# Performance work log

Hardware: AMD Instinct MI355X
Metric: run time of the kernel (lower is better)

The kernel has to match this reference:

```python
import jax, jax.numpy as jnp
import numpy as np

ALPHA_U = 1.0 / 10.0   # dt/tauu
ALPHA_V = 1.0 / 150.0  # dt/tauv
M = 10.0

def setup_inputs() -> dict:
    key = jax.random.key(0)
    ks = jax.random.split(key, 6)
    B, D_in, H = 8192, 1024, 2048
    stdv = 1.0 / np.sqrt(H)
    return {
        "x": jax.random.normal(ks[0], (B, D_in), dtype=jnp.float32),
        "u": jax.random.normal(ks[1], (B, H), dtype=jnp.float32),
        "v": jax.random.normal(ks[2], (B, H), dtype=jnp.float32),
        "win": jax.random.uniform(ks[3], (H, D_in), dtype=jnp.float32, minval=-stdv, maxval=stdv),
        "wr": jax.random.uniform(ks[4], (H, H), dtype=jnp.float32, minval=-stdv, maxval=stdv),
        "bias": jax.random.uniform(ks[5], (H,), dtype=jnp.float32, minval=-stdv, maxval=stdv),
    }

def reference(x, u, v, win, wr, bias):
    # v update: leaky blend toward m*u, then relu
    v_new = jax.nn.relu((1.0 - ALPHA_V) * v + (ALPHA_V * M) * u)
    # u update: leaky blend with input + recurrent drive minus adapted v
    drive = jnp.einsum('bi,hi->bh', x, win) + jnp.einsum('bk,hk->bh', u, wr) + bias - v_new
    u_new = jax.nn.relu((1.0 - ALPHA_U) * u + ALPHA_U * drive)
    return (u_new, v_new)
```

## Files before the change

kernel.cpp:

```cpp
#include <hip/hip_runtime.h>
#include <hip/hip_bf16.h>
#include <stdint.h>

#define B_DIM 8192
#define D_IN  1024
#define H_DIM 2048
#define K_DIM (D_IN + H_DIM)

#define CV_CONST  (1.0f - 1.0f/150.0f)
#define CUV_CONST (10.0f/150.0f)
#define CU_CONST  0.9f
#define AU_CONST  0.1f

typedef __attribute__((ext_vector_type(8))) short short8;
typedef __attribute__((ext_vector_type(4))) float floatx4;

__device__ __forceinline__ unsigned short f2bf(float f) {
    union { float f; unsigned u; } x; x.f = f;
    unsigned r = x.u + 0x7fffu + ((x.u >> 16) & 1u);
    return (unsigned short)(r >> 16);
}

#define N4_X   ((B_DIM * D_IN)  / 4)
#define N4_U   ((B_DIM * H_DIM) / 4)
#define N4_WIN ((H_DIM * D_IN)  / 4)
#define N4_WR  ((H_DIM * H_DIM) / 4)
#define N4_TOT (N4_X + N4_U + N4_WIN + N4_WR)

__global__ __launch_bounds__(256)
void pack_all(const float4* __restrict__ x, const float4* __restrict__ u,
              const float4* __restrict__ win, const float4* __restrict__ wr,
              unsigned short* __restrict__ Abf, unsigned short* __restrict__ Wbf) {
    int i = blockIdx.x * 256 + threadIdx.x;
    const float4* src; unsigned short* dst; int shift, mask, coloff;
    if (i < N4_X)                    { src = x;   dst = Abf; shift = 10; mask = 1023; coloff = 0;    }
    else if (i < N4_X + N4_U)        { i -= N4_X; src = u;   dst = Abf; shift = 11; mask = 2047; coloff = D_IN; }
    else if (i < N4_X + N4_U + N4_WIN){ i -= N4_X + N4_U; src = win; dst = Wbf; shift = 10; mask = 1023; coloff = 0; }
    else                             { i -= N4_X + N4_U + N4_WIN; src = wr; dst = Wbf; shift = 11; mask = 2047; coloff = D_IN; }
    int idx = i << 2;
    int r = idx >> shift;
    int c = idx & mask;
    float4 f = src[i];
    ushort4 o;
    o.x = f2bf(f.x); o.y = f2bf(f.y); o.z = f2bf(f.z); o.w = f2bf(f.w);
    *(ushort4*)(dst + (size_t)r * K_DIM + coloff + c) = o;
}

#define GLOAD_LDS16(gp, lp)                                                          \
    __builtin_amdgcn_global_load_lds(                                                \
        (const __attribute__((address_space(1))) unsigned int*)(gp),                 \
        (__attribute__((address_space(3))) unsigned int*)(lp), 16, 0, 0)

#define VMCNT(n)  asm volatile("s_waitcnt vmcnt(" #n ")" ::: "memory")
#define LGKM0     asm volatile("s_waitcnt lgkmcnt(0)" ::: "memory")
#define SCHEDB    __builtin_amdgcn_sched_barrier(0)
#define BAR       __builtin_amdgcn_s_barrier()
#define PRIO1     __builtin_amdgcn_s_setprio(1)
#define PRIO0     __builtin_amdgcn_s_setprio(0)

#define NT (K_DIM / 64)

#define ALO 0
#define BLO 16384
#define BHI 32768
#define AHI 49152

#define ES_STRIDE 68
#define ES_REGION (16 * ES_STRIDE)

__global__ __launch_bounds__(512, 2)
void gemm_fused(const unsigned short* __restrict__ A,
                const unsigned short* __restrict__ Wc,
                const float* __restrict__ u_in,
                const float* __restrict__ v_in,
                const float* __restrict__ bias,
                float* __restrict__ out)
{
    __shared__ __align__(16) unsigned char smem[131072];

    const int tid  = threadIdx.x;
    const int wave = tid >> 6;
    const int lane = tid & 63;
    const int wrh  = wave >> 2;
    const int wc   = wave & 3;

    const int bid   = blockIdx.x;
    const int xcd   = bid & 7;
    const int ord   = bid >> 3;
    const int tileM = ((xcd << 2) + (ord & 3)) << 8;
    const int tileN = (ord >> 2) << 8;

    const int frow = lane & 15;
    const int g    = lane >> 4;

    const unsigned short* Ag = A  + (size_t)(tileM + (wave >> 1) * 16 + frow) * K_DIM
                                  + (wave & 1) * 32 + g * 8;
    const unsigned short* Bg = Wc + (size_t)(tileN + (wave >> 2) * 64 + ((wave >> 1) & 1) * 16 + frow) * K_DIM
                                  + (wave & 1) * 32 + g * 8;
    const size_t R128 = (size_t)128 * K_DIM;
    const size_t R64  = (size_t) 64 * K_DIM;
    const size_t R32  = (size_t) 32 * K_DIM;

    const int w1024 = wave << 10;

    const int aRd = (wrh << 13) + (lane << 4);
    const int bRd = (wc  << 12) + (lane << 4);

    GLOAD_LDS16(Ag,               smem + ALO + w1024);
    GLOAD_LDS16(Ag + R128,        smem + ALO + 8192 + w1024);
    GLOAD_LDS16(Bg,               smem + BLO + w1024);
    GLOAD_LDS16(Bg + R128,        smem + BLO + 8192 + w1024);
    GLOAD_LDS16(Bg + R32,         smem + BHI + w1024);
    GLOAD_LDS16(Bg + R32 + R128,  smem + BHI + 8192 + w1024);
    GLOAD_LDS16(Ag + R64,         smem + AHI + w1024);
    GLOAD_LDS16(Ag + R64 + R128,  smem + AHI + 8192 + w1024);

    VMCNT(4);
    BAR;
    LGKM0;

    floatx4 acc[8][4] = {};
    short8 Ar[4][2], Bl[2][2], Bh[2][2];

#define RD_A(cb, unit, i2s) (*(const short8*)(smem + (cb) + (unit) + aRd + (i2s) * 1024))
#define RD_B(cb, unit, j2s) (*(const short8*)(smem + (cb) + (unit) + bRd + (j2s) * 1024))

#pragma clang loop unroll(disable)
    for (int t = 0; t < NT - 1; ++t) {
        const int cb = (t & 1) << 16;
        const int nb = cb ^ 65536;
        const size_t kk = (size_t)(t + 1) * 64;

        GLOAD_LDS16(Ag + kk,        smem + nb + ALO + w1024);
        GLOAD_LDS16(Ag + kk + R128, smem + nb + ALO + 8192 + w1024);
#pragma unroll
        for (int i = 0; i < 4; ++i) { Ar[i][0] = RD_A(cb, ALO, i*2); Ar[i][1] = RD_A(cb, ALO, i*2+1); }
#pragma unroll
        for (int j = 0; j < 2; ++j) { Bl[j][0] = RD_B(cb, BLO, j*2); Bl[j][1] = RD_B(cb, BLO, j*2+1); }
        VMCNT(4);
        BAR; LGKM0; SCHEDB;
        PRIO1;
#pragma unroll
        for (int i = 0; i < 4; ++i)
#pragma unroll
            for (int j = 0; j < 2; ++j) {
                acc[i][j] = __builtin_amdgcn_mfma_f32_16x16x32_bf16(Ar[i][0], Bl[j][0], acc[i][j], 0, 0, 0);
                acc[i][j] = __builtin_amdgcn_mfma_f32_16x16x32_bf16(Ar[i][1], Bl[j][1], acc[i][j], 0, 0, 0);
            }
        PRIO0; SCHEDB; BAR;

        GLOAD_LDS16(Bg + kk,        smem + nb + BLO + w1024);
        GLOAD_LDS16(Bg + kk + R128, smem + nb + BLO + 8192 + w1024);
#pragma unroll
        for (int j = 0; j < 2; ++j) { Bh[j][0] = RD_B(cb, BHI, j*2); Bh[j][1] = RD_B(cb, BHI, j*2+1); }
        VMCNT(4);
        BAR; LGKM0; SCHEDB;
        PRIO1;
#pragma unroll
        for (int i = 0; i < 4; ++i)
#pragma unroll
            for (int j = 0; j < 2; ++j) {
                acc[i][2+j] = __builtin_amdgcn_mfma_f32_16x16x32_bf16(Ar[i][0], Bh[j][0], acc[i][2+j], 0, 0, 0);
                acc[i][2+j] = __builtin_amdgcn_mfma_f32_16x16x32_bf16(Ar[i][1], Bh[j][1], acc[i][2+j], 0, 0, 0);
            }
        PRIO0; SCHEDB; BAR;

        GLOAD_LDS16(Bg + kk + R32,        smem + nb + BHI + w1024);
        GLOAD_LDS16(Bg + kk + R32 + R128, smem + nb + BHI + 8192 + w1024);
#pragma unroll
        for (int i = 0; i < 4; ++i) { Ar[i][0] = RD_A(cb, AHI, i*2); Ar[i][1] = RD_A(cb, AHI, i*2+1); }
        BAR; LGKM0; SCHEDB;
        PRIO1;
#pragma unroll
        for (int i = 0; i < 4; ++i)
#pragma unroll
            for (int j = 0; j < 2; ++j) {
                acc[4+i][2+j] = __builtin_amdgcn_mfma_f32_16x16x32_bf16(Ar[i][0], Bh[j][0], acc[4+i][2+j], 0, 0, 0);
                acc[4+i][2+j] = __builtin_amdgcn_mfma_f32_16x16x32_bf16(Ar[i][1], Bh[j][1], acc[4+i][2+j], 0, 0, 0);
            }
        PRIO0; SCHEDB; BAR;

        GLOAD_LDS16(Ag + kk + R64,        smem + nb + AHI + w1024);
        GLOAD_LDS16(Ag + kk + R64 + R128, smem + nb + AHI + 8192 + w1024);
        VMCNT(4);
        BAR; LGKM0; SCHEDB;
        PRIO1;
#pragma unroll
        for (int i = 0; i < 4; ++i)
#pragma unroll
            for (int j = 0; j < 2; ++j) {
                acc[4+i][j] = __builtin_amdgcn_mfma_f32_16x16x32_bf16(Ar[i][0], Bl[j][0], acc[4+i][j], 0, 0, 0);
                acc[4+i][j] = __builtin_amdgcn_mfma_f32_16x16x32_bf16(Ar[i][1], Bl[j][1], acc[4+i][j], 0, 0, 0);
            }
        PRIO0; SCHEDB; BAR;
    }

    {
        const int cb = ((NT - 1) & 1) << 16;
#pragma unroll
        for (int i = 0; i < 4; ++i) { Ar[i][0] = RD_A(cb, ALO, i*2); Ar[i][1] = RD_A(cb, ALO, i*2+1); }
#pragma unroll
        for (int j = 0; j < 2; ++j) { Bl[j][0] = RD_B(cb, BLO, j*2); Bl[j][1] = RD_B(cb, BLO, j*2+1); }
        VMCNT(2);
        BAR; LGKM0; SCHEDB;
        PRIO1;
#pragma unroll
        for (int i = 0; i < 4; ++i)
#pragma unroll
            for (int j = 0; j < 2; ++j) {
                acc[i][j] = __builtin_amdgcn_mfma_f32_16x16x32_bf16(Ar[i][0], Bl[j][0], acc[i][j], 0, 0, 0);
                acc[i][j] = __builtin_amdgcn_mfma_f32_16x16x32_bf16(Ar[i][1], Bl[j][1], acc[i][j], 0, 0, 0);
            }
        PRIO0; SCHEDB; BAR;
#pragma unroll
        for (int j = 0; j < 2; ++j) { Bh[j][0] = RD_B(cb, BHI, j*2); Bh[j][1] = RD_B(cb, BHI, j*2+1); }
        VMCNT(0);
        BAR; LGKM0; SCHEDB;
        PRIO1;
#pragma unroll
        for (int i = 0; i < 4; ++i)
#pragma unroll
            for (int j = 0; j < 2; ++j) {
                acc[i][2+j] = __builtin_amdgcn_mfma_f32_16x16x32_bf16(Ar[i][0], Bh[j][0], acc[i][2+j], 0, 0, 0);
                acc[i][2+j] = __builtin_amdgcn_mfma_f32_16x16x32_bf16(Ar[i][1], Bh[j][1], acc[i][2+j], 0, 0, 0);
            }
        PRIO0; SCHEDB; BAR;
#pragma unroll
        for (int i = 0; i < 4; ++i) { Ar[i][0] = RD_A(cb, AHI, i*2); Ar[i][1] = RD_A(cb, AHI, i*2+1); }
        BAR; LGKM0; SCHEDB;
        PRIO1;
#pragma unroll
        for (int i = 0; i < 4; ++i)
#pragma unroll
            for (int j = 0; j < 2; ++j) {
                acc[4+i][2+j] = __builtin_amdgcn_mfma_f32_16x16x32_bf16(Ar[i][0], Bh[j][0], acc[4+i][2+j], 0, 0, 0);
                acc[4+i][2+j] = __builtin_amdgcn_mfma_f32_16x16x32_bf16(Ar[i][1], Bh[j][1], acc[4+i][2+j], 0, 0, 0);
            }
        PRIO0; SCHEDB; BAR;
        PRIO1;
#pragma unroll
        for (int i = 0; i < 4; ++i)
#pragma unroll
            for (int j = 0; j < 2; ++j) {
                acc[4+i][j] = __builtin_amdgcn_mfma_f32_16x16x32_bf16(Ar[i][0], Bl[j][0], acc[4+i][j], 0, 0, 0);
                acc[4+i][j] = __builtin_amdgcn_mfma_f32_16x16x32_bf16(Ar[i][1], Bl[j][1], acc[4+i][j], 0, 0, 0);
            }
        PRIO0;
    }

    __syncthreads();

    float* Esf = (float*)smem;
    const int q    = lane >> 4;
    const int c16  = lane & 15;
    const int colg = tileN + wc * 64 + c16 * 4;
    const float4 b4 = *(const float4*)&bias[colg];
    const size_t outV = (size_t)B_DIM * H_DIM;

#pragma unroll
    for (int i = 0; i < 8; ++i) {
        float* Es = Esf + (wave * 2 + (i & 1)) * ES_REGION;
#pragma unroll
        for (int j = 0; j < 4; ++j)
#pragma unroll
            for (int r = 0; r < 4; ++r)
                Es[(q * 4 + r) * ES_STRIDE + j * 16 + c16] = acc[i][j][r];
#pragma unroll
        for (int rg = 0; rg < 4; rg++) {
            const int rloc = rg * 4 + q;
            const float4 a4 = *(const float4*)&Es[rloc * ES_STRIDE + c16 * 4];
            const size_t idx = (size_t)(tileM + wrh * 128 + i * 16 + rloc) * H_DIM + colg;
            const float4 u4 = *(const float4*)&u_in[idx];
            const float4 v4 = *(const float4*)&v_in[idx];
            float4 vn, un;
            vn.x = fmaxf(CV_CONST * v4.x + CUV_CONST * u4.x, 0.0f);
            vn.y = fmaxf(CV_CONST * v4.y + CUV_CONST * u4.y, 0.0f);
            vn.z = fmaxf(CV_CONST * v4.z + CUV_CONST * u4.z, 0.0f);
            vn.w = fmaxf(CV_CONST * v4.w + CUV_CONST * u4.w, 0.0f);
            un.x = fmaxf(CU_CONST * u4.x + AU_CONST * (a4.x + b4.x - vn.x), 0.0f);
            un.y = fmaxf(CU_CONST * u4.y + AU_CONST * (a4.y + b4.y - vn.y), 0.0f);
            un.z = fmaxf(CU_CONST * u4.z + AU_CONST * (a4.z + b4.z - vn.z), 0.0f);
            un.w = fmaxf(CU_CONST * u4.w + AU_CONST * (a4.w + b4.w - vn.w), 0.0f);
            *(float4*)&out[idx]        = un;
            *(float4*)&out[outV + idx] = vn;
        }
    }
}

extern "C" void kernel_launch(void* const* d_in, const int* in_sizes, int n_in,
                              void* d_out, int out_size, void* d_ws, size_t ws_size,
                              hipStream_t stream) {
    const float* x    = (const float*)d_in[0];
    const float* u    = (const float*)d_in[1];
    const float* v    = (const float*)d_in[2];
    const float* win  = (const float*)d_in[3];
    const float* wr   = (const float*)d_in[4];
    const float* bias = (const float*)d_in[5];
    float* out = (float*)d_out;

    unsigned short* Abf = (unsigned short*)d_ws;
    unsigned short* Wbf = Abf + (size_t)B_DIM * K_DIM;

    pack_all<<<N4_TOT / 256, 256, 0, stream>>>(
        (const float4*)x, (const float4*)u, (const float4*)win, (const float4*)wr,
        Abf, Wbf);

    gemm_fused<<<256, 512, 0, stream>>>(Abf, Wbf, u, v, bias, out);
}
```

Before: 371.1 us.

## Shrink GEMM block tile from 256x256 to 128x128 with 4 waves

Reduces the fused GEMM tile from 256x256 with 8 waves to 128x128 with 4 waves per block. LDS drops to 64KB and the grid grows from 256 to 1024 blocks, remapped across XCDs. The goal is better occupancy and load balance across CUs, since 256 blocks barely fills the GPU. The cost is lower arithmetic intensity per block and more global/L2 traffic for A and B tiles.

```diff
diff --git a/kernel.cpp b/kernel.cpp
--- a/kernel.cpp
+++ b/kernel.cpp
@@ -61,14 +61,14 @@
 #define NT (K_DIM / 64)
 
 #define ALO 0
-#define BLO 16384
-#define BHI 32768
-#define AHI 49152
+#define BLO 8192
+#define BHI 16384
+#define AHI 24576
 
 #define ES_STRIDE 68
 #define ES_REGION (16 * ES_STRIDE)
 
-__global__ __launch_bounds__(512, 2)
+__global__ __launch_bounds__(256, 2)
 void gemm_fused(const unsigned short* __restrict__ A,
                 const unsigned short* __restrict__ Wc,
                 const float* __restrict__ u_in,
@@ -76,72 +76,71 @@
                 const float* __restrict__ bias,
                 float* __restrict__ out)
 {
-    __shared__ __align__(16) unsigned char smem[131072];
+    __shared__ __align__(16) unsigned char smem[65536];
 
     const int tid  = threadIdx.x;
     const int wave = tid >> 6;
     const int lane = tid & 63;
-    const int wrh  = wave >> 2;
-    const int wc   = wave & 3;
+    const int wrh  = wave >> 1;
+    const int wc   = wave & 1;
 
     const int bid   = blockIdx.x;
-    const int xcd   = bid & 7;
-    const int ord   = bid >> 3;
-    const int tileM = ((xcd << 2) + (ord & 3)) << 8;
-    const int tileN = (ord >> 2) << 8;
+    const int wid   = ((bid & 7) << 7) | (bid >> 3);
+    const int tileMr = (wid >> 4) << 7;
+    const int tileNr = (wid & 15) << 7;
 
     const int frow = lane & 15;
     const int g    = lane >> 4;
 
-    const unsigned short* Ag = A  + (size_t)(tileM + (wave >> 1) * 16 + frow) * K_DIM
+    const unsigned short* Ag = A  + (size_t)(tileMr + (wave >> 1) * 16 + frow) * K_DIM
                                   + (wave & 1) * 32 + g * 8;
-    const unsigned short* Bg = Wc + (size_t)(tileN + (wave >> 2) * 64 + ((wave >> 1) & 1) * 16 + frow) * K_DIM
+    const unsigned short* Bg = Wc + (size_t)(tileNr + (wave >> 1) * 16 + frow) * K_DIM
                                   + (wave & 1) * 32 + g * 8;
-    const size_t R128 = (size_t)128 * K_DIM;
-    const size_t R64  = (size_t) 64 * K_DIM;
-    const size_t R32  = (size_t) 32 * K_DIM;
+    const size_t R96 = (size_t)96 * K_DIM;
+    const size_t R64 = (size_t)64 * K_DIM;
+    const size_t R32 = (size_t)32 * K_DIM;
 
     const int w1024 = wave << 10;
 
-    const int aRd = (wrh << 13) + (lane << 4);
+    const int aRd = (wrh << 12) + (lane << 4);
     const int bRd = (wc  << 12) + (lane << 4);
 
-    GLOAD_LDS16(Ag,               smem + ALO + w1024);
-    GLOAD_LDS16(Ag + R128,        smem + ALO + 8192 + w1024);
-    GLOAD_LDS16(Bg,               smem + BLO + w1024);
-    GLOAD_LDS16(Bg + R128,        smem + BLO + 8192 + w1024);
-    GLOAD_LDS16(Bg + R32,         smem + BHI + w1024);
-    GLOAD_LDS16(Bg + R32 + R128,  smem + BHI + 8192 + w1024);
-    GLOAD_LDS16(Ag + R64,         smem + AHI + w1024);
-    GLOAD_LDS16(Ag + R64 + R128,  smem + AHI + 8192 + w1024);
+    GLOAD_LDS16(Ag,        smem + ALO + w1024);
+    GLOAD_LDS16(Ag + R64,  smem + ALO + 4096 + w1024);
+    GLOAD_LDS16(Bg,        smem + BLO + w1024);
+    GLOAD_LDS16(Bg + R64,  smem + BLO + 4096 + w1024);
+    GLOAD_LDS16(Bg + R32,  smem + BHI + w1024);
+    GLOAD_LDS16(Bg + R96,  smem + BHI + 4096 + w1024);
+    GLOAD_LDS16(Ag + R32,  smem + AHI + w1024);
+    GLOAD_LDS16(Ag + R96,  smem + AHI + 4096 + w1024);
 
     VMCNT(4);
     BAR;
     LGKM0;
 
-    floatx4 acc[8][4] = {};
-    short8 Ar[4][2], Bl[2][2], Bh[2][2];
+    floatx4 acc[4][4] = {};
+    short8 Ar[2][2], Bl[2][2], Bh[2][2];
 
 #define RD_A(cb, unit, i2s) (*(const short8*)(smem + (cb) + (unit) + aRd + (i2s) * 1024))
 #define RD_B(cb, unit, j2s) (*(const short8*)(smem + (cb) + (unit) + bRd + (j2s) * 1024))
 
 #pragma clang loop unroll(disable)
     for (int t = 0; t < NT - 1; ++t) {
-        const int cb = (t & 1) << 16;
-        const int nb = cb ^ 65536;
+        const int cb = (t & 1) << 15;
+        const int nb = cb ^ 32768;
         const size_t kk = (size_t)(t + 1) * 64;
 
-        GLOAD_LDS16(Ag + kk,        smem + nb + ALO + w1024);
-        GLOAD_LDS16(Ag + kk + R128, smem + nb + ALO + 8192 + w1024);
-#pragma unroll
-        for (int i = 0; i < 4; ++i) { Ar[i][0] = RD_A(cb, ALO, i*2); Ar[i][1] = RD_A(cb, ALO, i*2+1); }
+        GLOAD_LDS16(Ag + kk,       smem + nb + ALO + w1024);
+        GLOAD_LDS16(Ag + kk + R64, smem + nb + ALO + 4096 + w1024);
+#pragma unroll
+        for (int i = 0; i < 2; ++i) { Ar[i][0] = RD_A(cb, ALO, i*2); Ar[i][1] = RD_A(cb, ALO, i*2+1); }
 #pragma unroll
         for (int j = 0; j < 2; ++j) { Bl[j][0] = RD_B(cb, BLO, j*2); Bl[j][1] = RD_B(cb, BLO, j*2+1); }
         VMCNT(4);
         BAR; LGKM0; SCHEDB;
         PRIO1;
 #pragma unroll
-        for (int i = 0; i < 4; ++i)
+        for (int i = 0; i < 2; ++i)
 #pragma unroll
             for (int j = 0; j < 2; ++j) {
                 acc[i][j] = __builtin_amdgcn_mfma_f32_16x16x32_bf16(Ar[i][0], Bl[j][0], acc[i][j], 0, 0, 0);
@@ -149,15 +148,15 @@
             }
         PRIO0; SCHEDB; BAR;
 
-        GLOAD_LDS16(Bg + kk,        smem + nb + BLO + w1024);
-        GLOAD_LDS16(Bg + kk + R128, smem + nb + BLO + 8192 + w1024);
+        GLOAD_LDS16(Bg + kk,       smem + nb + BLO + w1024);
+        GLOAD_LDS16(Bg + kk + R64, smem + nb + BLO + 4096 + w1024);
 #pragma unroll
         for (int j = 0; j < 2; ++j) { Bh[j][0] = RD_B(cb, BHI, j*2); Bh[j][1] = RD_B(cb, BHI, j*2+1); }
         VMCNT(4);
         BAR; LGKM0; SCHEDB;
         PRIO1;
 #pragma unroll
-        for (int i = 0; i < 4; ++i)
+        for (int i = 0; i < 2; ++i)
 #pragma unroll
             for (int j = 0; j < 2; ++j) {
                 acc[i][2+j] = __builtin_amdgcn_mfma_f32_16x16x32_bf16(Ar[i][0], Bh[j][0], acc[i][2+j], 0, 0, 0);
@@ -165,47 +164,47 @@
             }
         PRIO0; SCHEDB; BAR;
 
-        GLOAD_LDS16(Bg + kk + R32,        smem + nb + BHI + w1024);
-        GLOAD_LDS16(Bg + kk + R32 + R128, smem + nb + BHI + 8192 + w1024);
-#pragma unroll
-        for (int i = 0; i < 4; ++i) { Ar[i][0] = RD_A(cb, AHI, i*2); Ar[i][1] = RD_A(cb, AHI, i*2+1); }
-        BAR; LGKM0; SCHEDB;
-        PRIO1;
-#pragma unroll
-        for (int i = 0; i < 4; ++i)
-#pragma unroll
-            for (int j = 0; j < 2; ++j) {
-                acc[4+i][2+j] = __builtin_amdgcn_mfma_f32_16x16x32_bf16(Ar[i][0], Bh[j][0], acc[4+i][2+j], 0, 0, 0);
-                acc[4+i][2+j] = __builtin_amdgcn_mfma_f32_16x16x32_bf16(Ar[i][1], Bh[j][1], acc[4+i][2+j], 0, 0, 0);
-            }
-        PRIO0; SCHEDB; BAR;
-
-        GLOAD_LDS16(Ag + kk + R64,        smem + nb + AHI + w1024);
-        GLOAD_LDS16(Ag + kk + R64 + R128, smem + nb + AHI + 8192 + w1024);
+        GLOAD_LDS16(Bg + kk + R32, smem + nb + BHI + w1024);
+        GLOAD_LDS16(Bg + kk + R96, smem + nb + BHI + 4096 + w1024);
+#pragma unroll
+        for (int i = 0; i < 2; ++i) { Ar[i][0] = RD_A(cb, AHI, i*2); Ar[i][1] = RD_A(cb, AHI, i*2+1); }
+        BAR; LGKM0; SCHEDB;
+        PRIO1;
+#pragma unroll
+        for (int i = 0; i < 2; ++i)
+#pragma unroll
+            for (int j = 0; j < 2; ++j) {
+                acc[2+i][2+j] = __builtin_amdgcn_mfma_f32_16x16x32_bf16(Ar[i][0], Bh[j][0], acc[2+i][2+j], 0, 0, 0);
+                acc[2+i][2+j] = __builtin_amdgcn_mfma_f32_16x16x32_bf16(Ar[i][1], Bh[j][1], acc[2+i][2+j], 0, 0, 0);
+            }
+        PRIO0; SCHEDB; BAR;
+
+        GLOAD_LDS16(Ag + kk + R32, smem + nb + AHI + w1024);
+        GLOAD_LDS16(Ag + kk + R96, smem + nb + AHI + 4096 + w1024);
         VMCNT(4);
         BAR; LGKM0; SCHEDB;
         PRIO1;
 #pragma unroll
-        for (int i = 0; i < 4; ++i)
-#pragma unroll
-            for (int j = 0; j < 2; ++j) {
-                acc[4+i][j] = __builtin_amdgcn_mfma_f32_16x16x32_bf16(Ar[i][0], Bl[j][0], acc[4+i][j], 0, 0, 0);
-                acc[4+i][j] = __builtin_amdgcn_mfma_f32_16x16x32_bf16(Ar[i][1], Bl[j][1], acc[4+i][j], 0, 0, 0);
+        for (int i = 0; i < 2; ++i)
+#pragma unroll
+            for (int j = 0; j < 2; ++j) {
+                acc[2+i][j] = __builtin_amdgcn_mfma_f32_16x16x32_bf16(Ar[i][0], Bl[j][0], acc[2+i][j], 0, 0, 0);
+                acc[2+i][j] = __builtin_amdgcn_mfma_f32_16x16x32_bf16(Ar[i][1], Bl[j][1], acc[2+i][j], 0, 0, 0);
             }
         PRIO0; SCHEDB; BAR;
     }
 
     {
-        const int cb = ((NT - 1) & 1) << 16;
-#pragma unroll
-        for (int i = 0; i < 4; ++i) { Ar[i][0] = RD_A(cb, ALO, i*2); Ar[i][1] = RD_A(cb, ALO, i*2+1); }
+        const int cb = ((NT - 1) & 1) << 15;
+#pragma unroll
+        for (int i = 0; i < 2; ++i) { Ar[i][0] = RD_A(cb, ALO, i*2); Ar[i][1] = RD_A(cb, ALO, i*2+1); }
 #pragma unroll
         for (int j = 0; j < 2; ++j) { Bl[j][0] = RD_B(cb, BLO, j*2); Bl[j][1] = RD_B(cb, BLO, j*2+1); }
         VMCNT(2);
         BAR; LGKM0; SCHEDB;
         PRIO1;
 #pragma unroll
-        for (int i = 0; i < 4; ++i)
+        for (int i = 0; i < 2; ++i)
 #pragma unroll
             for (int j = 0; j < 2; ++j) {
                 acc[i][j] = __builtin_amdgcn_mfma_f32_16x16x32_bf16(Ar[i][0], Bl[j][0], acc[i][j], 0, 0, 0);
@@ -218,7 +217,7 @@
         BAR; LGKM0; SCHEDB;
         PRIO1;
 #pragma unroll
-        for (int i = 0; i < 4; ++i)
+        for (int i = 0; i < 2; ++i)
 #pragma unroll
             for (int j = 0; j < 2; ++j) {
                 acc[i][2+j] = __builtin_amdgcn_mfma_f32_16x16x32_bf16(Ar[i][0], Bh[j][0], acc[i][2+j], 0, 0, 0);
@@ -226,24 +225,24 @@
             }
         PRIO0; SCHEDB; BAR;
 #pragma unroll
-        for (int i = 0; i < 4; ++i) { Ar[i][0] = RD_A(cb, AHI, i*2); Ar[i][1] = RD_A(cb, AHI, i*2+1); }
-        BAR; LGKM0; SCHEDB;
-        PRIO1;
-#pragma unroll
-        for (int i = 0; i < 4; ++i)
-#pragma unroll
-            for (int j = 0; j < 2; ++j) {
-                acc[4+i][2+j] = __builtin_amdgcn_mfma_f32_16x16x32_bf16(Ar[i][0], Bh[j][0], acc[4+i][2+j], 0, 0, 0);
-                acc[4+i][2+j] = __builtin_amdgcn_mfma_f32_16x16x32_bf16(Ar[i][1], Bh[j][1], acc[4+i][2+j], 0, 0, 0);
-            }
-        PRIO0; SCHEDB; BAR;
-        PRIO1;
-#pragma unroll
-        for (int i = 0; i < 4; ++i)
-#pragma unroll
-            for (int j = 0; j < 2; ++j) {
-                acc[4+i][j] = __builtin_amdgcn_mfma_f32_16x16x32_bf16(Ar[i][0], Bl[j][0], acc[4+i][j], 0, 0, 0);
-                acc[4+i][j] = __builtin_amdgcn_mfma_f32_16x16x32_bf16(Ar[i][1], Bl[j][1], acc[4+i][j], 0, 0, 0);
+        for (int i = 0; i < 2; ++i) { Ar[i][0] = RD_A(cb, AHI, i*2); Ar[i][1] = RD_A(cb, AHI, i*2+1); }
+        BAR; LGKM0; SCHEDB;
+        PRIO1;
+#pragma unroll
+        for (int i = 0; i < 2; ++i)
+#pragma unroll
+            for (int j = 0; j < 2; ++j) {
+                acc[2+i][2+j] = __builtin_amdgcn_mfma_f32_16x16x32_bf16(Ar[i][0], Bh[j][0], acc[2+i][2+j], 0, 0, 0);
+                acc[2+i][2+j] = __builtin_amdgcn_mfma_f32_16x16x32_bf16(Ar[i][1], Bh[j][1], acc[2+i][2+j], 0, 0, 0);
+            }
+        PRIO0; SCHEDB; BAR;
+        PRIO1;
+#pragma unroll
+        for (int i = 0; i < 2; ++i)
+#pragma unroll
+            for (int j = 0; j < 2; ++j) {
+                acc[2+i][j] = __builtin_amdgcn_mfma_f32_16x16x32_bf16(Ar[i][0], Bl[j][0], acc[2+i][j], 0, 0, 0);
+                acc[2+i][j] = __builtin_amdgcn_mfma_f32_16x16x32_bf16(Ar[i][1], Bl[j][1], acc[2+i][j], 0, 0, 0);
             }
         PRIO0;
     }
@@ -253,12 +252,12 @@
     float* Esf = (float*)smem;
     const int q    = lane >> 4;
     const int c16  = lane & 15;
-    const int colg = tileN + wc * 64 + c16 * 4;
+    const int colg = tileNr + wc * 64 + c16 * 4;
     const float4 b4 = *(const float4*)&bias[colg];
     const size_t outV = (size_t)B_DIM * H_DIM;
 
 #pragma unroll
-    for (int i = 0; i < 8; ++i) {
+    for (int i = 0; i < 4; ++i) {
         float* Es = Esf + (wave * 2 + (i & 1)) * ES_REGION;
 #pragma unroll
         for (int j = 0; j < 4; ++j)
@@ -269,7 +268,7 @@
         for (int rg = 0; rg < 4; rg++) {
             const int rloc = rg * 4 + q;
             const float4 a4 = *(const float4*)&Es[rloc * ES_STRIDE + c16 * 4];
-            const size_t idx = (size_t)(tileM + wrh * 128 + i * 16 + rloc) * H_DIM + colg;
+            const size_t idx = (size_t)(tileMr + wrh * 64 + i * 16 + rloc) * H_DIM + colg;
             const float4 u4 = *(const float4*)&u_in[idx];
             const float4 v4 = *(const float4*)&v_in[idx];
             float4 vn, un;
@@ -305,5 +304,5 @@
         (const float4*)x, (const float4*)u, (const float4*)win, (const float4*)wr,
         Abf, Wbf);
 
-    gemm_fused<<<256, 512, 0, stream>>>(Abf, Wbf, u, v, bias, out);
+    gemm_fused<<<1024, 256, 0, stream>>>(Abf, Wbf, u, v, bias, out);
 }
```

Result: slower. 451.7 us (+21.7%).
